# Optimization experiments

Measured on AMD Instinct MI355X. Metric: run time of the kernel, lower is better.

## Reference

```python
import jax, jax.numpy as jnp
import numpy as np

N_EXPERTS = 8
TOPK = 2
D_MODEL = 1024
D_FF = 4096

def setup_inputs() -> dict:
    key = jax.random.key(0)
    k_x, k_g, k_1, k_2 = jax.random.split(key, 4)
    x = jax.random.normal(k_x, (4, 2048, D_MODEL), dtype=jnp.float32)
    Wg = jax.random.normal(k_g, (D_MODEL, N_EXPERTS), dtype=jnp.float32) * 0.02
    W1 = jax.random.normal(k_1, (N_EXPERTS, D_MODEL, D_FF), dtype=jnp.float32) * 0.02
    W2 = jax.random.normal(k_2, (N_EXPERTS, D_FF, D_MODEL), dtype=jnp.float32) * 0.02
    return {"x": x, "Wg": Wg, "W1": W1, "W2": W2}

def reference(x, Wg, W1, W2):
    B, S, D = x.shape
    xt = x.reshape(-1, D)                      # [T, D]
    T = xt.shape[0]
    logits = xt @ Wg                            # [T, E]
    vals, idx = jax.lax.top_k(logits, TOPK)     # [T, K]
    w = jax.nn.softmax(vals, axis=-1)           # renormalize over selected experts
    # scatter top-k weights into dense [T, E] gate matrix (zeros elsewhere)
    gates = jnp.zeros((T, N_EXPERTS), dtype=x.dtype).at[jnp.arange(T)[:, None], idx].set(w)
    out = jnp.zeros_like(xt)
    for e in range(N_EXPERTS):                  # fixed small loop over experts
        h = jax.nn.silu(xt @ W1[e]) @ W2[e]     # [T, D]
        out = out + gates[:, e:e+1] * h
    return out.reshape(B, S, D)
```

## Files before the change

kernel.cpp:

```cpp
#include <hip/hip_runtime.h>
#include <hip/hip_bf16.h>
#include <math.h>

#define T_TOK 8192
#define DM 1024
#define DF 4096
#define NE 8
#define MAXT 144

typedef __attribute__((ext_vector_type(4))) float  f32x4;
typedef __attribute__((ext_vector_type(8))) short  s16x8;
typedef __attribute__((ext_vector_type(8))) unsigned short u16x8;
typedef __attribute__((ext_vector_type(4))) unsigned short u16x4;

__device__ __forceinline__ unsigned short f2bf(float f) {
    unsigned int u = __builtin_bit_cast(unsigned int, f);
    u = (u + 0x7FFFu + ((u >> 16) & 1u)) >> 16;
    return (unsigned short)u;
}

#define GLDS16(gptr, lptr)                                                         \
    __builtin_amdgcn_global_load_lds(                                              \
        (const __attribute__((address_space(1))) void*)(gptr),                     \
        (__attribute__((address_space(3))) void*)(lptr), 16, 0, 0)

#define BAR() asm volatile("s_barrier" ::: "memory")

template<int W>
__device__ __forceinline__ void waitvm() {
    if constexpr (W == 4)      asm volatile("s_waitcnt vmcnt(4)" ::: "memory");
    else                       asm volatile("s_waitcnt vmcnt(0)" ::: "memory");
}

__global__ __launch_bounds__(256) void route_kernel(
    const float* __restrict__ x, const float* __restrict__ Wg,
    int* __restrict__ counts, int* __restrict__ lists, float* __restrict__ pw,
    unsigned short* __restrict__ xb)
{
    int tok  = (int)((blockIdx.x * blockDim.x + threadIdx.x) >> 6);
    int lane = threadIdx.x & 63;
    if (tok >= T_TOK) return;

    const float* xr = x + (size_t)tok * DM;
    float acc[NE];
#pragma unroll
    for (int e = 0; e < NE; ++e) acc[e] = 0.f;

    for (int i = lane; i < DM; i += 64) {
        float xv = xr[i];
        const float* wr = Wg + (size_t)i * NE;
#pragma unroll
        for (int e = 0; e < NE; ++e) acc[e] += xv * wr[e];
    }

    if (xb) {
        unsigned short* xrow = xb + (size_t)tok * DM;
#pragma unroll
        for (int i = lane * 4; i < DM; i += 256) {
            float4 v = *reinterpret_cast<const float4*>(xr + i);
            u16x4 o;
            o[0] = f2bf(v.x); o[1] = f2bf(v.y); o[2] = f2bf(v.z); o[3] = f2bf(v.w);
            *reinterpret_cast<u16x4*>(xrow + i) = o;
        }
    }

#pragma unroll
    for (int e = 0; e < NE; ++e) {
#pragma unroll
        for (int off = 32; off > 0; off >>= 1)
            acc[e] += __shfl_xor(acc[e], off, 64);
    }

    if (lane == 0) {
        int i0 = 0; float v0 = acc[0];
#pragma unroll
        for (int e = 1; e < NE; ++e) if (acc[e] > v0) { v0 = acc[e]; i0 = e; }
        int i1 = -1; float v1 = -INFINITY;
#pragma unroll
        for (int e = 0; e < NE; ++e) if (e != i0 && acc[e] > v1) { v1 = acc[e]; i1 = e; }
        float e1 = __expf(v1 - v0);
        float s  = 1.f + e1;
        int p0 = tok * 2, p1 = tok * 2 + 1;
        pw[p0] = 1.f / s;
        pw[p1] = e1 / s;
        int pos0 = atomicAdd(&counts[i0], 1);
        lists[i0 * T_TOK + pos0] = p0;
        int pos1 = atomicAdd(&counts[i1], 1);
        lists[i1 * T_TOK + pos1] = p1;
    }
}

__global__ void offsets_kernel(const int* __restrict__ counts, int* __restrict__ offsets,
                               unsigned* __restrict__ table, int* __restrict__ ntp)
{
    if (threadIdx.x == 0) {
        int s = 0, ti = 0;
        for (int e = 0; e < NE; ++e) {
            offsets[e] = s;
            int cnt = counts[e];
            for (int t0 = 0; t0 < cnt; t0 += 128)
                table[ti++] = ((unsigned)e << 20) | (unsigned)t0;
            s += cnt;
        }
        ntp[0] = ti;
        for (; ti < MAXT; ++ti) table[ti] = 0xFFFFFFFFu;
    }
}

template<int K, int N>
__global__ __launch_bounds__(256) void transpose_conv_kernel(
    const float* __restrict__ W, unsigned short* __restrict__ Wt)
{
    int e  = blockIdx.z;
    int k0 = blockIdx.x * 64;
    int n0 = blockIdx.y * 64;
    const float* We = W + (size_t)e * K * N;
    unsigned short* Wte = Wt + (size_t)e * K * N;

    __shared__ unsigned short t[64][73];
    int c4 = (threadIdx.x & 15) * 4;
    int r  = threadIdx.x >> 4;
#pragma unroll
    for (int i = 0; i < 4; ++i) {
        int rr = r + i * 16;
        float4 v = *reinterpret_cast<const float4*>(We + (size_t)(k0 + rr) * N + n0 + c4);
        t[rr][c4 + 0] = f2bf(v.x); t[rr][c4 + 1] = f2bf(v.y);
        t[rr][c4 + 2] = f2bf(v.z); t[rr][c4 + 3] = f2bf(v.w);
    }
    __syncthreads();
    int kc = (threadIdx.x & 7) * 8;
    int rn = threadIdx.x >> 3;
#pragma unroll
    for (int i = 0; i < 2; ++i) {
        int nn = rn + i * 32;
        u16x8 o;
#pragma unroll
        for (int j = 0; j < 8; ++j) o[j] = t[kc + j][nn];
        *reinterpret_cast<u16x8*>(Wte + (size_t)(n0 + nn) * K + k0 + kc) = o;
    }
}

template<int N, int K, int SPLITK, bool IS_G1>
__global__ __launch_bounds__(256, 4) void moe_gemm12(
    const unsigned short* __restrict__ A,
    const unsigned short* __restrict__ Wt,
    const int* __restrict__ counts, const int* __restrict__ offsets,
    const int* __restrict__ lists, const unsigned* __restrict__ table,
    const int* __restrict__ ntp, const float* __restrict__ pw,
    unsigned short* __restrict__ Hout, float* __restrict__ Oout)
{
    constexpr int NT  = N / 128;
    constexpr int PAN = NT * SPLITK;
    constexpr int KS  = K / SPLITK;
    constexpr int NC  = KS / 32;
    static_assert(NC >= 4, "pipeline depth");

    __shared__ __attribute__((aligned(16))) char lds[32768];

    int ntl  = ntp[0];
    int live = ntl * PAN;
    int orig = blockIdx.x;
    if (orig >= live) return;
    int q = live >> 3, r = live & 7;
    int xq = orig & 7, ib = orig >> 3;
    int work = (xq < r ? xq * (q + 1) : r * (q + 1) + (xq - r) * q) + ib;
    int rt    = work / PAN;
    int panel = work - rt * PAN;
    int nt    = panel >> (SPLITK - 1);
    int sk    = panel & (SPLITK - 1);
    int koff  = sk * KS;

    unsigned te = table[rt];
    int e     = (int)(te >> 20);
    int slot0 = (int)(te & 0xFFFFFu);
    int cnt   = counts[e];
    int off   = offsets[e];
    int ntile = nt * 128;

    int tid  = threadIdx.x;
    int lane = tid & 63;
    int wid  = tid >> 6;
    int wm = wid >> 1;
    int wn = wid & 1;
    int l15 = lane & 15, l4 = lane >> 4;

    const unsigned short* Be = Wt + (size_t)e * N * K;

    int ssw = ((tid & 3) ^ ((tid >> 3) & 3)) * 8;
    int r0  = tid >> 2;
    unsigned aOff0, aOff1;
    {
#pragma unroll
        for (int u = 0; u < 2; ++u) {
            int sl = slot0 + u * 64 + r0;
            unsigned grow;
            if (IS_G1) grow = (sl < cnt) ? (unsigned)(lists[e * T_TOK + sl] >> 1) : 0u;
            else       grow = (unsigned)(off + ((sl < cnt) ? sl : slot0));
            unsigned v = grow * (unsigned)K + (unsigned)(koff + ssw);
            if (u == 0) aOff0 = v; else aOff1 = v;
        }
    }
    unsigned bOff0 = (unsigned)(ntile + r0)      * (unsigned)K + (unsigned)(koff + ssw);
    unsigned bOff1 = (unsigned)(ntile + 64 + r0) * (unsigned)K + (unsigned)(koff + ssw);

    auto stage = [&](int s, int c) {
        int ko = c * 32;
        char* dA = lds + s * 8192 + tid * 16;
        char* dB = lds + 16384 + s * 8192 + tid * 16;
        GLDS16(A + aOff0 + ko, dA);
        GLDS16(A + aOff1 + ko, dA + 4096);
        GLDS16(Be + bOff0 + ko, dB);
        GLDS16(Be + bOff1 + ko, dB + 4096);
    };

    int swzb = (l4 ^ ((l15 >> 1) & 3)) * 16;
    int aRd = (wm * 64 + l15) * 64 + swzb;
    int bRd = (wn * 64 + l15) * 64 + swzb;

    f32x4 acc[4][4];
#pragma unroll
    for (int m = 0; m < 4; ++m)
#pragma unroll
        for (int n = 0; n < 4; ++n) acc[m][n] = (f32x4){0.f, 0.f, 0.f, 0.f};

    auto compute = [&](int s) {
        const char* Ab = lds + s * 8192;
        const char* Bb = lds + 16384 + s * 8192;
        s16x8 af[4];
#pragma unroll
        for (int m = 0; m < 4; ++m)
            af[m] = *reinterpret_cast<const s16x8*>(Ab + aRd + m * 1024);
        __builtin_amdgcn_s_setprio(1);
#pragma unroll
        for (int n = 0; n < 4; ++n) {
            s16x8 bf = *reinterpret_cast<const s16x8*>(Bb + bRd + n * 1024);
#pragma unroll
            for (int m = 0; m < 4; ++m)
                acc[m][n] = __builtin_amdgcn_mfma_f32_16x16x32_bf16(af[m], bf, acc[m][n], 0, 0, 0);
        }
        __builtin_amdgcn_s_setprio(0);
    };

    stage(0, 0); stage(1, 1);
    for (int c = 0; c < NC; ++c) {
        if (c + 1 < NC) waitvm<4>();
        else            waitvm<0>();
        BAR();
        compute(c & 1);
        BAR();
        if (c + 2 < NC) stage(c & 1, c + 2);
    }

#pragma unroll
    for (int m = 0; m < 4; ++m) {
        int trow = wm * 64 + m * 16 + l4 * 4;
#pragma unroll
        for (int rr = 0; rr < 4; ++rr) {
            int slot = slot0 + trow + rr;
            if (slot >= cnt) continue;
            if (IS_G1) {
                unsigned short* hr = Hout + (size_t)(off + slot) * N;
#pragma unroll
                for (int n = 0; n < 4; ++n) {
                    int col = ntile + wn * 64 + n * 16 + l15;
                    float v = acc[m][n][rr];
                    float s = v / (1.f + __expf(-v));
                    hr[col] = f2bf(s);
                }
            } else {
                int p = lists[e * T_TOK + slot];
                float w = pw[p];
                float* orow = Oout + (size_t)(p >> 1) * DM;
#pragma unroll
                for (int n = 0; n < 4; ++n) {
                    int col = ntile + wn * 64 + n * 16 + l15;
                    atomicAdd(orow + col, w * acc[m][n][rr]);
                }
            }
        }
    }
}

#define BMF 16
#define BFF 256
__global__ __launch_bounds__(256) void expert_gemm_f32(
    const float* __restrict__ x, const float* __restrict__ W1, const float* __restrict__ W2,
    const int* __restrict__ counts, const int* __restrict__ lists, const float* __restrict__ pw,
    float* __restrict__ out)
{
    int e    = blockIdx.y;
    int tile = blockIdx.x;
    int cnt  = counts[e];
    int start = tile * BMF;
    if (start >= cnt) return;

    __shared__ float xs[BMF][DM];
    __shared__ float hs[BMF][BFF];
    __shared__ int   toks[BMF];
    __shared__ float wgt[BMF];

    int tid = threadIdx.x;
    int nm  = cnt - start; if (nm > BMF) nm = BMF;

    if (tid < BMF) {
        if (tid < nm) {
            int p = lists[e * T_TOK + start + tid];
            toks[tid] = p >> 1;
            wgt[tid]  = pw[p];
        } else { toks[tid] = -1; wgt[tid] = 0.f; }
    }
    __syncthreads();
    for (int m = 0; m < BMF; ++m) {
        int t = toks[m];
        const float* xr = (t >= 0) ? (x + (size_t)t * DM) : nullptr;
        for (int i = tid; i < DM; i += 256) xs[m][i] = (t >= 0) ? xr[i] : 0.f;
    }
    __syncthreads();

    const float* W1e = W1 + (size_t)e * DM * DF;
    const float* W2e = W2 + (size_t)e * DF * DM;
    float acc[BMF][4];
#pragma unroll
    for (int m = 0; m < BMF; ++m)
#pragma unroll
        for (int c = 0; c < 4; ++c) acc[m][c] = 0.f;

    for (int fc = 0; fc < DF; fc += BFF) {
        float hacc[BMF];
#pragma unroll
        for (int m = 0; m < BMF; ++m) hacc[m] = 0.f;
        const float* w1col = W1e + fc + tid;
#pragma unroll 4
        for (int i = 0; i < DM; ++i) {
            float w1v = w1col[(size_t)i * DF];
#pragma unroll
            for (int m = 0; m < BMF; ++m) hacc[m] += xs[m][i] * w1v;
        }
        __syncthreads();
#pragma unroll
        for (int m = 0; m < BMF; ++m) {
            float v = hacc[m];
            hs[m][tid] = v / (1.f + __expf(-v));
        }
        __syncthreads();
        const float* w2base = W2e + (size_t)fc * DM + tid * 4;
        for (int f = 0; f < BFF; ++f) {
            float4 w2v = *reinterpret_cast<const float4*>(w2base + (size_t)f * DM);
#pragma unroll
            for (int m = 0; m < BMF; ++m) {
                float h = hs[m][f];
                acc[m][0] += h * w2v.x; acc[m][1] += h * w2v.y;
                acc[m][2] += h * w2v.z; acc[m][3] += h * w2v.w;
            }
        }
        __syncthreads();
    }
    int c0 = tid * 4;
#pragma unroll
    for (int m = 0; m < BMF; ++m) {
        int t = toks[m];
        if (t < 0) continue;
        float w = wgt[m];
        float* op = out + (size_t)t * DM + c0;
        atomicAdd(op + 0, w * acc[m][0]);
        atomicAdd(op + 1, w * acc[m][1]);
        atomicAdd(op + 2, w * acc[m][2]);
        atomicAdd(op + 3, w * acc[m][3]);
    }
}

extern "C" void kernel_launch(void* const* d_in, const int* in_sizes, int n_in,
                              void* d_out, int out_size, void* d_ws, size_t ws_size,
                              hipStream_t stream)
{
    const float* x  = (const float*)d_in[0];
    const float* Wg = (const float*)d_in[1];
    const float* W1 = (const float*)d_in[2];
    const float* W2 = (const float*)d_in[3];
    float* out = (float*)d_out;

    char* ws = (char*)d_ws;
    int*      counts  = (int*)(ws + 0);
    int*      offsets = (int*)(ws + 64);
    int*      ntp     = (int*)(ws + 128);
    unsigned* table   = (unsigned*)(ws + 256);
    int*      lists   = (int*)(ws + 2048);
    float*    pw      = (float*)(ws + 2048 + 262144);

    const size_t o_xb  = 524288;
    const size_t sz_xb = (size_t)T_TOK * DM * 2;
    const size_t o_w1t = o_xb + sz_xb;
    const size_t sz_w  = (size_t)NE * DM * DF * 2;
    const size_t o_w2t = o_w1t + sz_w;
    const size_t o_h   = o_w2t + sz_w;
    const size_t sz_h  = (size_t)(2 * T_TOK) * DF * 2;
    const size_t NEEDED = o_h + sz_h;

    bool fast = (ws_size >= NEEDED);
    unsigned short* xb = fast ? (unsigned short*)(ws + o_xb) : nullptr;

    hipMemsetAsync(counts, 0, 64, stream);
    route_kernel<<<T_TOK / 4, 256, 0, stream>>>(x, Wg, counts, lists, pw, xb);

    if (fast) {
        unsigned short* w1t = (unsigned short*)(ws + o_w1t);
        unsigned short* w2t = (unsigned short*)(ws + o_w2t);
        unsigned short* H   = (unsigned short*)(ws + o_h);

        hipMemsetAsync(d_out, 0, (size_t)out_size * sizeof(float), stream);
        offsets_kernel<<<1, 64, 0, stream>>>(counts, offsets, table, ntp);
        {
            dim3 g(DM / 64, DF / 64, NE);
            transpose_conv_kernel<DM, DF><<<g, 256, 0, stream>>>(W1, w1t);
        }
        {
            dim3 g(DF / 64, DM / 64, NE);
            transpose_conv_kernel<DF, DM><<<g, 256, 0, stream>>>(W2, w2t);
        }
        moe_gemm12<DF, DM, 1, true><<<dim3(MAXT * 32), 256, 0, stream>>>(
            xb, w1t, counts, offsets, lists, table, ntp, pw, H, nullptr);
        moe_gemm12<DM, DF, 2, false><<<dim3(MAXT * 16), 256, 0, stream>>>(
            H, w2t, counts, offsets, lists, table, ntp, pw, nullptr, out);
    } else {
        hipMemsetAsync(d_out, 0, (size_t)out_size * sizeof(float), stream);
        dim3 grid(T_TOK / BMF, NE);
        expert_gemm_f32<<<grid, 256, 0, stream>>>(x, W1, W2, counts, lists, pw, out);
    }
}
```

Measured before the change: 712.6 us.

## Deepen GEMM K-chunk to 64 with single-barrier pipeline, fuse output zeroing and transposes

The expert GEMMs now stage 64-wide K chunks into a 64 KB double buffer with an 8-way XOR swizzle, and run one wait and barrier per chunk instead of two. Occupancy is lowered to 2 blocks per SM to fit the larger LDS footprint. Zeroing the output moves into the routing kernel in place of a separate memset, and the two weight transpose launches merge into one. This aims to cut barrier and launch overhead, at the cost of less latency hiding from fewer resident blocks and a prefetch distance of only one chunk.

```diff
diff --git a/kernel.cpp b/kernel.cpp
--- a/kernel.cpp
+++ b/kernel.cpp
@@ -24,19 +24,23 @@
         (const __attribute__((address_space(1))) void*)(gptr),                     \
         (__attribute__((address_space(3))) void*)(lptr), 16, 0, 0)
 
-#define BAR() asm volatile("s_barrier" ::: "memory")
-
-template<int W>
-__device__ __forceinline__ void waitvm() {
-    if constexpr (W == 4)      asm volatile("s_waitcnt vmcnt(4)" ::: "memory");
-    else                       asm volatile("s_waitcnt vmcnt(0)" ::: "memory");
-}
+#define BAR()  asm volatile("s_barrier" ::: "memory")
+#define SBAR() __builtin_amdgcn_sched_barrier(0)
+#define VM0()  asm volatile("s_waitcnt vmcnt(0)" ::: "memory")
 
 __global__ __launch_bounds__(256) void route_kernel(
     const float* __restrict__ x, const float* __restrict__ Wg,
     int* __restrict__ counts, int* __restrict__ lists, float* __restrict__ pw,
-    unsigned short* __restrict__ xb)
-{
+    unsigned short* __restrict__ xb, float* __restrict__ outz)
+{
+    {
+        size_t base = ((size_t)blockIdx.x * 256 + threadIdx.x) * 16;
+        float4 z = {0.f, 0.f, 0.f, 0.f};
+#pragma unroll
+        for (int j = 0; j < 4; ++j)
+            *reinterpret_cast<float4*>(outz + base + j * 4) = z;
+    }
+
     int tok  = (int)((blockIdx.x * blockDim.x + threadIdx.x) >> 6);
     int lane = threadIdx.x & 63;
     if (tok >= T_TOK) return;
@@ -107,22 +111,31 @@
     }
 }
 
-template<int K, int N>
-__global__ __launch_bounds__(256) void transpose_conv_kernel(
-    const float* __restrict__ W, unsigned short* __restrict__ Wt)
-{
-    int e  = blockIdx.z;
-    int k0 = blockIdx.x * 64;
-    int n0 = blockIdx.y * 64;
+__global__ __launch_bounds__(256) void transpose_conv_all(
+    const float* __restrict__ W1, const float* __restrict__ W2,
+    unsigned short* __restrict__ w1t, unsigned short* __restrict__ w2t)
+{
+    int id = blockIdx.x;
+    const float* W; unsigned short* Wt; int K, N, e, k0, n0;
+    if (id < 8192) {
+        W = W1; Wt = w1t; K = DM; N = DF;
+        e = id >> 10; int r = id & 1023;
+        k0 = (r & 15) * 64; n0 = (r >> 4) * 64;
+    } else {
+        id -= 8192;
+        W = W2; Wt = w2t; K = DF; N = DM;
+        e = id >> 10; int r = id & 1023;
+        k0 = (r >> 4) * 64; n0 = (r & 15) * 64;
+    }
     const float* We = W + (size_t)e * K * N;
     unsigned short* Wte = Wt + (size_t)e * K * N;
 
     __shared__ unsigned short t[64][73];
     int c4 = (threadIdx.x & 15) * 4;
-    int r  = threadIdx.x >> 4;
+    int rr0 = threadIdx.x >> 4;
 #pragma unroll
     for (int i = 0; i < 4; ++i) {
-        int rr = r + i * 16;
+        int rr = rr0 + i * 16;
         float4 v = *reinterpret_cast<const float4*>(We + (size_t)(k0 + rr) * N + n0 + c4);
         t[rr][c4 + 0] = f2bf(v.x); t[rr][c4 + 1] = f2bf(v.y);
         t[rr][c4 + 2] = f2bf(v.z); t[rr][c4 + 3] = f2bf(v.w);
@@ -141,7 +154,7 @@
 }
 
 template<int N, int K, int SPLITK, bool IS_G1>
-__global__ __launch_bounds__(256, 4) void moe_gemm12(
+__global__ __launch_bounds__(256, 2) void moe_gemm13(
     const unsigned short* __restrict__ A,
     const unsigned short* __restrict__ Wt,
     const int* __restrict__ counts, const int* __restrict__ offsets,
@@ -152,10 +165,10 @@
     constexpr int NT  = N / 128;
     constexpr int PAN = NT * SPLITK;
     constexpr int KS  = K / SPLITK;
-    constexpr int NC  = KS / 32;
-    static_assert(NC >= 4, "pipeline depth");
-
-    __shared__ __attribute__((aligned(16))) char lds[32768];
+    constexpr int NC  = KS / 64;
+    static_assert(NC >= 2, "pipeline depth");
+
+    __shared__ __attribute__((aligned(16))) char lds[65536];
 
     int ntl  = ntp[0];
     int live = ntl * PAN;
@@ -186,36 +199,32 @@
 
     const unsigned short* Be = Wt + (size_t)e * N * K;
 
-    int ssw = ((tid & 3) ^ ((tid >> 3) & 3)) * 8;
-    int r0  = tid >> 2;
-    unsigned aOff0, aOff1;
-    {
-#pragma unroll
-        for (int u = 0; u < 2; ++u) {
-            int sl = slot0 + u * 64 + r0;
-            unsigned grow;
-            if (IS_G1) grow = (sl < cnt) ? (unsigned)(lists[e * T_TOK + sl] >> 1) : 0u;
-            else       grow = (unsigned)(off + ((sl < cnt) ? sl : slot0));
-            unsigned v = grow * (unsigned)K + (unsigned)(koff + ssw);
-            if (u == 0) aOff0 = v; else aOff1 = v;
-        }
-    }
-    unsigned bOff0 = (unsigned)(ntile + r0)      * (unsigned)K + (unsigned)(koff + ssw);
-    unsigned bOff1 = (unsigned)(ntile + 64 + r0) * (unsigned)K + (unsigned)(koff + ssw);
+    int g8 = ((tid & 7) ^ ((tid >> 3) & 7)) * 8;
+    int r0 = tid >> 3;
+    unsigned aOff[4], bOff[4];
+#pragma unroll
+    for (int u = 0; u < 4; ++u) {
+        int sl = slot0 + u * 32 + r0;
+        unsigned grow;
+        if (IS_G1) grow = (sl < cnt) ? (unsigned)(lists[e * T_TOK + sl] >> 1) : 0u;
+        else       grow = (unsigned)(off + ((sl < cnt) ? sl : slot0));
+        aOff[u] = grow * (unsigned)K + (unsigned)(koff + g8);
+        bOff[u] = (unsigned)(ntile + u * 32 + r0) * (unsigned)K + (unsigned)(koff + g8);
+    }
 
     auto stage = [&](int s, int c) {
-        int ko = c * 32;
-        char* dA = lds + s * 8192 + tid * 16;
-        char* dB = lds + 16384 + s * 8192 + tid * 16;
-        GLDS16(A + aOff0 + ko, dA);
-        GLDS16(A + aOff1 + ko, dA + 4096);
-        GLDS16(Be + bOff0 + ko, dB);
-        GLDS16(Be + bOff1 + ko, dB + 4096);
+        int ko = c * 64;
+        char* dA = lds + s * 16384 + tid * 16;
+        char* dB = lds + 32768 + s * 16384 + tid * 16;
+#pragma unroll
+        for (int u = 0; u < 4; ++u) GLDS16(A + aOff[u] + ko, dA + u * 4096);
+#pragma unroll
+        for (int u = 0; u < 4; ++u) GLDS16(Be + bOff[u] + ko, dB + u * 4096);
     };
 
-    int swzb = (l4 ^ ((l15 >> 1) & 3)) * 16;
-    int aRd = (wm * 64 + l15) * 64 + swzb;
-    int bRd = (wn * 64 + l15) * 64 + swzb;
+    int swz = (l4 ^ (l15 & 7)) * 16;
+    int aRd = wm * 8192 + l15 * 128 + swz;
+    int bRd = wn * 8192 + l15 * 128 + swz;
 
     f32x4 acc[4][4];
 #pragma unroll
@@ -224,31 +233,38 @@
         for (int n = 0; n < 4; ++n) acc[m][n] = (f32x4){0.f, 0.f, 0.f, 0.f};
 
     auto compute = [&](int s) {
-        const char* Ab = lds + s * 8192;
-        const char* Bb = lds + 16384 + s * 8192;
-        s16x8 af[4];
-#pragma unroll
-        for (int m = 0; m < 4; ++m)
-            af[m] = *reinterpret_cast<const s16x8*>(Ab + aRd + m * 1024);
-        __builtin_amdgcn_s_setprio(1);
-#pragma unroll
-        for (int n = 0; n < 4; ++n) {
-            s16x8 bf = *reinterpret_cast<const s16x8*>(Bb + bRd + n * 1024);
+        const char* Ab = lds + s * 16384;
+        const char* Bb = lds + 32768 + s * 16384;
+#pragma unroll
+        for (int ks = 0; ks < 2; ++ks) {
+            const int x = ks * 64;
+            s16x8 af[4], bf[4];
 #pragma unroll
             for (int m = 0; m < 4; ++m)
-                acc[m][n] = __builtin_amdgcn_mfma_f32_16x16x32_bf16(af[m], bf, acc[m][n], 0, 0, 0);
-        }
-        __builtin_amdgcn_s_setprio(0);
+                af[m] = *reinterpret_cast<const s16x8*>(Ab + ((aRd + m * 2048) ^ x));
+#pragma unroll
+            for (int n = 0; n < 4; ++n)
+                bf[n] = *reinterpret_cast<const s16x8*>(Bb + ((bRd + n * 2048) ^ x));
+            __builtin_amdgcn_s_setprio(1);
+#pragma unroll
+            for (int n = 0; n < 4; ++n)
+#pragma unroll
+                for (int m = 0; m < 4; ++m)
+                    acc[m][n] = __builtin_amdgcn_mfma_f32_16x16x32_bf16(
+                        af[m], bf[n], acc[m][n], 0, 0, 0);
+            __builtin_amdgcn_s_setprio(0);
+        }
     };
 
-    stage(0, 0); stage(1, 1);
+    stage(0, 0);
+    VM0(); BAR();
+    int cur = 0;
     for (int c = 0; c < NC; ++c) {
-        if (c + 1 < NC) waitvm<4>();
-        else            waitvm<0>();
-        BAR();
-        compute(c & 1);
-        BAR();
-        if (c + 2 < NC) stage(c & 1, c + 2);
+        if (c + 1 < NC) stage(cur ^ 1, c + 1);
+        compute(cur);
+        SBAR();
+        VM0(); BAR();
+        cur ^= 1;
     }
 
 #pragma unroll
@@ -400,29 +416,20 @@
     unsigned short* xb = fast ? (unsigned short*)(ws + o_xb) : nullptr;
 
     hipMemsetAsync(counts, 0, 64, stream);
-    route_kernel<<<T_TOK / 4, 256, 0, stream>>>(x, Wg, counts, lists, pw, xb);
+    route_kernel<<<T_TOK / 4, 256, 0, stream>>>(x, Wg, counts, lists, pw, xb, out);
 
     if (fast) {
         unsigned short* w1t = (unsigned short*)(ws + o_w1t);
         unsigned short* w2t = (unsigned short*)(ws + o_w2t);
         unsigned short* H   = (unsigned short*)(ws + o_h);
 
-        hipMemsetAsync(d_out, 0, (size_t)out_size * sizeof(float), stream);
         offsets_kernel<<<1, 64, 0, stream>>>(counts, offsets, table, ntp);
-        {
-            dim3 g(DM / 64, DF / 64, NE);
-            transpose_conv_kernel<DM, DF><<<g, 256, 0, stream>>>(W1, w1t);
-        }
-        {
-            dim3 g(DF / 64, DM / 64, NE);
-            transpose_conv_kernel<DF, DM><<<g, 256, 0, stream>>>(W2, w2t);
-        }
-        moe_gemm12<DF, DM, 1, true><<<dim3(MAXT * 32), 256, 0, stream>>>(
+        transpose_conv_all<<<16384, 256, 0, stream>>>(W1, W2, w1t, w2t);
+        moe_gemm13<DF, DM, 1, true><<<dim3(MAXT * 32), 256, 0, stream>>>(
             xb, w1t, counts, offsets, lists, table, ntp, pw, H, nullptr);
-        moe_gemm12<DM, DF, 2, false><<<dim3(MAXT * 16), 256, 0, stream>>>(
+        moe_gemm13<DM, DF, 2, false><<<dim3(MAXT * 16), 256, 0, stream>>>(
             H, w2t, counts, offsets, lists, table, ntp, pw, nullptr, out);
     } else {
-        hipMemsetAsync(d_out, 0, (size_t)out_size * sizeof(float), stream);
         dim3 grid(T_TOK / BMF, NE);
         expert_gemm_f32<<<grid, 256, 0, stream>>>(x, W1, W2, counts, lists, pw, out);
     }
```

Result: slower. 754.5 us (+5.9%).
